# Optimization experiments

Hardware: AMD Instinct MI355X
Metric: run time of the kernel (lower is better)

Reference implementation:

```python
import jax, jax.numpy as jnp
import numpy as np

ROPE_BASE = 10000.0

def _rms_norm(x):
    eps = jnp.asarray(jnp.finfo(x.dtype).eps, x.dtype)
    return x * jax.lax.rsqrt(jnp.mean(x * x, axis=-1, keepdims=True) + eps)

def _rope(x):
    # x: [B, S, H, hd]; rotate-halves variant: y1 = x1*cos + x2*sin, y2 = -x1*sin + x2*cos
    S, hd = x.shape[1], x.shape[3]
    d = hd // 2
    inv_freq = 1.0 / (ROPE_BASE ** (jnp.arange(0, hd, 2, dtype=jnp.float32) / hd))  # [d]
    t = jnp.arange(S, dtype=jnp.float32)
    freqs = jnp.outer(t, inv_freq)                       # [S, d]
    cos = jnp.cos(freqs)[None, :, None, :].astype(x.dtype)
    sin = jnp.sin(freqs)[None, :, None, :].astype(x.dtype)
    x1, x2 = x[..., :d], x[..., d:]
    return jnp.concatenate([x1 * cos + x2 * sin, -x1 * sin + x2 * cos], axis=-1)

def setup_inputs() -> dict:
    key = jax.random.key(0)
    ks = jax.random.split(key, 7)
    B, S, D = 1, 2048, 1024
    std = 0.02
    return {
        "x": jax.random.normal(ks[0], (B, S, D), jnp.float32),
        "v1": jax.random.normal(ks[1], (B, S, D), jnp.float32),
        "Wq": jax.random.normal(ks[2], (D, D), jnp.float32) * std,
        "Wk": jax.random.normal(ks[3], (D, D), jnp.float32) * std,
        "Wv": jax.random.normal(ks[4], (D, D), jnp.float32) * std,
        "Wout": jax.random.normal(ks[5], (D, D), jnp.float32) * std,
        "lambdas": jnp.float32(0.5),
        "n_heads": 16,
    }

def reference(x, v1, Wq, Wk, Wv, Wout, lambdas, n_heads):
    B, S, D = x.shape
    H = n_heads
    hd = D // H
    # QKV projections (CastedLinear, no bias)
    q = (x @ Wq.T).reshape(B, S, H, hd)
    k = (x @ Wk.T).reshape(B, S, H, hd)
    v = (x @ Wv.T).reshape(B, S, H, hd)
    # value residual mix with first-layer values v1
    v = (1.0 - lambdas) * v + lambdas * v1.reshape(B, S, H, hd)
    # per-head RMS norm (no learned scale) then RoPE
    q, k = _rms_norm(q), _rms_norm(k)
    q, k = _rope(q), _rope(k)
    # causal attention (flex_attention default: softmax, scale 1/sqrt(hd))
    scale = 1.0 / jnp.sqrt(jnp.asarray(hd, x.dtype))
    scores = jnp.einsum('bqhd,bkhd->bhqk', q, k) * scale        # [B,H,S,S]
    causal = jnp.tril(jnp.ones((S, S), dtype=bool))
    scores = jnp.where(causal[None, None], scores, jnp.asarray(-jnp.inf, scores.dtype))
    p = jax.nn.softmax(scores, axis=-1)
    y = jnp.einsum('bhqk,bkhd->bqhd', p, v).reshape(B, S, D)
    y = y @ Wout.T
    return (y, v1)
```

## Files before the change

kernel.cpp:

```cpp
#include <hip/hip_runtime.h>
#include <hip/hip_bf16.h>

#define S_LEN 2048
#define D_DIM 1024
#define NH    16
#define NEG_BIG (-1.0e30f)

#define EPI_NORMROPE 1
#define EPI_VMIX_T   2
#define EPI_F32      3

typedef __attribute__((ext_vector_type(8))) short bf16x8;
typedef __attribute__((ext_vector_type(4))) float f32x4;
typedef const __attribute__((address_space(1))) unsigned char gu8_t;
typedef __attribute__((address_space(3))) unsigned char lu8_t;

__device__ __forceinline__ float bf2f(unsigned short h) {
    union { unsigned int u; float f; } v; v.u = ((unsigned int)h) << 16; return v.f;
}
__device__ __forceinline__ unsigned short f2b(float f) {
    union { float f; unsigned int u; } v; v.f = f;
    unsigned int u = v.u;
    return (unsigned short)((u + 0x7FFFu + ((u >> 16) & 1u)) >> 16);
}

__global__ __launch_bounds__(256)
void to_bf16(const float* __restrict__ x,  const float* __restrict__ wq,
             const float* __restrict__ wk, const float* __restrict__ wv,
             const float* __restrict__ wo,
             unsigned short* __restrict__ xb,  unsigned short* __restrict__ wqb,
             unsigned short* __restrict__ wkb, unsigned short* __restrict__ wvb,
             unsigned short* __restrict__ wob)
{
    const int z = blockIdx.y;
    const float* s; unsigned short* d; int n;
    switch (z) {
        case 0: s = x;  d = xb;  n = S_LEN * D_DIM; break;
        case 1: s = wq; d = wqb; n = D_DIM * D_DIM; break;
        case 2: s = wk; d = wkb; n = D_DIM * D_DIM; break;
        case 3: s = wv; d = wvb; n = D_DIM * D_DIM; break;
        default: s = wo; d = wob; n = D_DIM * D_DIM; break;
    }
    int i8 = blockIdx.x * 256 + threadIdx.x;
    if (i8 * 8 >= n) return;
    const float* sp = s + (size_t)i8 * 8;
    float4 lo = *(const float4*)sp, hi = *(const float4*)(sp + 4);
    uint4 p;
    p.x = f2b(lo.x) | ((unsigned)f2b(lo.y) << 16);
    p.y = f2b(lo.z) | ((unsigned)f2b(lo.w) << 16);
    p.z = f2b(hi.x) | ((unsigned)f2b(hi.y) << 16);
    p.w = f2b(hi.z) | ((unsigned)f2b(hi.w) << 16);
    *(uint4*)(d + (size_t)i8 * 8) = p;
}

__global__ __launch_bounds__(256, 2)
void gemm_bt(const unsigned short* __restrict__ A,
             const unsigned short* __restrict__ B0, const unsigned short* __restrict__ B1,
             const unsigned short* __restrict__ B2,
             void* __restrict__ C0, void* __restrict__ C1, void* __restrict__ C2,
             const float* __restrict__ vmix, const float* __restrict__ lam,
             int epiPack)
{
    const int which = blockIdx.z;
    const unsigned short* Bp = (which == 0) ? B0 : ((which == 1) ? B1 : B2);
    void* C = (which == 0) ? C0 : ((which == 1) ? C1 : C2);
    const int epi = (epiPack >> (8 * which)) & 0xff;
    const int tn = blockIdx.x * 128;
    const int tm = blockIdx.y * 128;

    __shared__ unsigned short Asl[128 * 32];
    __shared__ unsigned short Bsl[128 * 32];

    const int t    = threadIdx.x;
    const int lane = t & 63;
    const int wave = t >> 6;
    const int wm   = (wave >> 1) * 64;
    const int wn   = (wave & 1) * 64;
    const int lrow = lane & 15;
    const int quad = lane >> 4;
    const int srow = lane >> 2;
    const int scol = (lane & 3) * 8;

    f32x4 acc[4][4];
    #pragma unroll
    for (int i = 0; i < 4; ++i)
        #pragma unroll
        for (int j = 0; j < 4; ++j) {
            f32x4 z = {0.f, 0.f, 0.f, 0.f};
            acc[i][j] = z;
        }

    for (int k0 = 0; k0 < D_DIM; k0 += 32) {
        #pragma unroll
        for (int rep = 0; rep < 2; ++rep) {
            int grp = wave * 2 + rep;
            int row = grp * 16 + srow;
            __builtin_amdgcn_global_load_lds(
                (gu8_t*)(A + (size_t)(tm + row) * D_DIM + k0 + scol),
                (lu8_t*)&Asl[grp * 512], 16, 0, 0);
            __builtin_amdgcn_global_load_lds(
                (gu8_t*)(Bp + (size_t)(tn + row) * D_DIM + k0 + scol),
                (lu8_t*)&Bsl[grp * 512], 16, 0, 0);
        }
        __syncthreads();
        bf16x8 af[4], bfr[4];
        #pragma unroll
        for (int i = 0; i < 4; ++i)
            af[i] = *(const bf16x8*)(&Asl[(wm + i * 16 + lrow) * 32 + quad * 8]);
        #pragma unroll
        for (int j = 0; j < 4; ++j)
            bfr[j] = *(const bf16x8*)(&Bsl[(wn + j * 16 + lrow) * 32 + quad * 8]);
        #pragma unroll
        for (int i = 0; i < 4; ++i)
            #pragma unroll
            for (int j = 0; j < 4; ++j)
                acc[i][j] = __builtin_amdgcn_mfma_f32_16x16x32_bf16(af[i], bfr[j], acc[i][j], 0, 0, 0);
        __syncthreads();
    }

    if (epi == EPI_NORMROPE) {
        #pragma unroll
        for (int i = 0; i < 4; ++i) {
            #pragma unroll
            for (int r = 0; r < 4; ++r) {
                int row = tm + wm + i * 16 + quad * 4 + r;
                float v0 = acc[i][0][r], v1 = acc[i][1][r];
                float v2 = acc[i][2][r], v3 = acc[i][3][r];
                float ss = v0 * v0 + v1 * v1 + v2 * v2 + v3 * v3;
                ss += __shfl_xor(ss, 1); ss += __shfl_xor(ss, 2);
                ss += __shfl_xor(ss, 4); ss += __shfl_xor(ss, 8);
                float rms = rsqrtf(ss * (1.f / 64.f) + 1.1920929e-7f);
                v0 *= rms; v1 *= rms; v2 *= rms; v3 *= rms;
                float fs = (float)row;
                float a0 = fs * exp2f(-0.41524101186092030f * (float)lrow);
                float a1 = fs * exp2f(-0.41524101186092030f * (float)(16 + lrow));
                float s0, c0, s1, c1;
                __sincosf(a0, &s0, &c0);
                __sincosf(a1, &s1, &c1);
                unsigned short* Cb = (unsigned short*)C;
                size_t base = (size_t)row * D_DIM + tn + wn + lrow;
                Cb[base]      = f2b(v0 * c0 + v2 * s0);
                Cb[base + 16] = f2b(v1 * c1 + v3 * s1);
                Cb[base + 32] = f2b(-v0 * s0 + v2 * c0);
                Cb[base + 48] = f2b(-v1 * s1 + v3 * c1);
            }
        }
    } else if (epi == EPI_VMIX_T) {
        float lamf = *lam;
        #pragma unroll
        for (int i = 0; i < 4; ++i) {
            int cm0 = tm + wm + i * 16 + quad * 4;
            #pragma unroll
            for (int j = 0; j < 4; ++j) {
                int cn = tn + wn + j * 16 + lrow;
                ushort4 pk;
                float vals[4];
                #pragma unroll
                for (int r = 0; r < 4; ++r) {
                    size_t idx = (size_t)(cm0 + r) * D_DIM + cn;
                    vals[r] = (1.f - lamf) * acc[i][j][r] + lamf * vmix[idx];
                }
                pk.x = f2b(vals[0]); pk.y = f2b(vals[1]);
                pk.z = f2b(vals[2]); pk.w = f2b(vals[3]);
                *(ushort4*)((unsigned short*)C + (size_t)cn * S_LEN + cm0) = pk;
            }
        }
    } else {
        #pragma unroll
        for (int i = 0; i < 4; ++i) {
            int cm0 = tm + wm + i * 16 + quad * 4;
            #pragma unroll
            for (int j = 0; j < 4; ++j) {
                int cn = tn + wn + j * 16 + lrow;
                #pragma unroll
                for (int r = 0; r < 4; ++r)
                    ((float*)C)[(size_t)(cm0 + r) * D_DIM + cn] = acc[i][j][r];
            }
        }
    }
}

__global__ __launch_bounds__(256, 2)
void attn_mfma(const unsigned short* Qb,
               const unsigned short* __restrict__ Kb,
               const unsigned short* __restrict__ Vtg,
               unsigned short* Ob)
{
    const int bx = blockIdx.x;
    const int qt = (bx & 1) ? (31 - (bx >> 1)) : (bx >> 1);
    const int h  = blockIdx.y;
    const int t  = threadIdx.x;
    const int w  = t >> 6;
    const int l  = t & 63;
    const int l15  = l & 15;
    const int quad = l >> 4;
    const int hco  = h * 64;

    __shared__ unsigned short Ks[64][72];
    __shared__ unsigned short Vt[64][72];
    __shared__ unsigned short Ps[4][16][72];

    const unsigned short* qrow = Qb + (size_t)(qt * 64 + w * 16 + l15) * D_DIM + hco;
    bf16x8 qf0 = *(const bf16x8*)(qrow + quad * 8);
    bf16x8 qf1 = *(const bf16x8*)(qrow + 32 + quad * 8);

    f32x4 oac[4];
    #pragma unroll
    for (int nt = 0; nt < 4; ++nt) { f32x4 z = {0.f,0.f,0.f,0.f}; oac[nt] = z; }
    float l_lane[4] = {0.f, 0.f, 0.f, 0.f};

    const int rr = t >> 2;
    const int dc = (t & 3) * 16;

    const unsigned short* kbase = Kb  + (size_t)rr * D_DIM + hco + dc;
    const unsigned short* vbase = Vtg + (size_t)(hco + rr) * S_LEN + dc;

    uint4 ka0, ka1, va0, va1;
    ka0 = *(const uint4*)kbase;  ka1 = *(const uint4*)(kbase + 8);
    va0 = *(const uint4*)vbase;  va1 = *(const uint4*)(vbase + 8);

    const int row_base = qt * 64 + w * 16 + quad * 4;

    for (int j = 0; j <= qt; ++j) {
        __syncthreads();
        *(uint4*)&Ks[rr][dc]     = ka0;
        *(uint4*)&Ks[rr][dc + 8] = ka1;
        *(uint4*)&Vt[rr][dc]     = va0;
        *(uint4*)&Vt[rr][dc + 8] = va1;
        __syncthreads();
        if (j < qt) {
            const unsigned short* kp = kbase + (size_t)(j + 1) * 64 * D_DIM;
            const unsigned short* vp = vbase + (size_t)(j + 1) * 64;
            ka0 = *(const uint4*)kp;  ka1 = *(const uint4*)(kp + 8);
            va0 = *(const uint4*)vp;  va1 = *(const uint4*)(vp + 8);
        }

        f32x4 sac[4];
        #pragma unroll
        for (int nt = 0; nt < 4; ++nt) {
            f32x4 z = {0.f,0.f,0.f,0.f};
            bf16x8 kf0 = *(const bf16x8*)&Ks[nt * 16 + l15][quad * 8];
            z = __builtin_amdgcn_mfma_f32_16x16x32_bf16(qf0, kf0, z, 0, 0, 0);
            bf16x8 kf1 = *(const bf16x8*)&Ks[nt * 16 + l15][32 + quad * 8];
            z = __builtin_amdgcn_mfma_f32_16x16x32_bf16(qf1, kf1, z, 0, 0, 0);
            sac[nt] = z;
        }

        #pragma unroll
        for (int nt = 0; nt < 4; ++nt) {
            int key_g = j * 64 + nt * 16 + l15;
            #pragma unroll
            for (int r = 0; r < 4; ++r) {
                float s = sac[nt][r] * 0.125f - 8.0f;
                if (key_g > row_base + r) s = NEG_BIG;
                float pe = __expf(s);
                l_lane[r] += pe;
                Ps[w][quad * 4 + r][nt * 16 + l15] = f2b(pe);
            }
        }

        bf16x8 pf0 = *(const bf16x8*)&Ps[w][l15][quad * 8];
        bf16x8 pf1 = *(const bf16x8*)&Ps[w][l15][32 + quad * 8];
        #pragma unroll
        for (int nt = 0; nt < 4; ++nt) {
            bf16x8 vf0 = *(const bf16x8*)&Vt[nt * 16 + l15][quad * 8];
            oac[nt] = __builtin_amdgcn_mfma_f32_16x16x32_bf16(pf0, vf0, oac[nt], 0, 0, 0);
            bf16x8 vf1 = *(const bf16x8*)&Vt[nt * 16 + l15][32 + quad * 8];
            oac[nt] = __builtin_amdgcn_mfma_f32_16x16x32_bf16(pf1, vf1, oac[nt], 0, 0, 0);
        }
    }

    float inv[4];
    #pragma unroll
    for (int r = 0; r < 4; ++r) {
        float lr = l_lane[r];
        #pragma unroll
        for (int d = 1; d < 16; d <<= 1) lr += __shfl_xor(lr, d);
        inv[r] = 1.f / lr;
    }
    #pragma unroll
    for (int nt = 0; nt < 4; ++nt) {
        #pragma unroll
        for (int r = 0; r < 4; ++r) {
            int row_g = row_base + r;
            Ob[(size_t)row_g * D_DIM + hco + nt * 16 + l15] = f2b(oac[nt][r] * inv[r]);
        }
    }
}

__global__ __launch_bounds__(256)
void copy_v1(const uint4* __restrict__ src, uint4* __restrict__ dst) {
    int i = blockIdx.x * 256 + threadIdx.x;
    dst[i] = src[i];
}

extern "C" void kernel_launch(void* const* d_in, const int* in_sizes, int n_in,
                              void* d_out, int out_size, void* d_ws, size_t ws_size,
                              hipStream_t stream)
{
    const float* x    = (const float*)d_in[0];
    const float* v1   = (const float*)d_in[1];
    const float* Wq   = (const float*)d_in[2];
    const float* Wk   = (const float*)d_in[3];
    const float* Wv   = (const float*)d_in[4];
    const float* Wout = (const float*)d_in[5];
    const float* lam  = (const float*)d_in[6];
    float* out = (float*)d_out;

    const size_t SD = (size_t)S_LEN * D_DIM;
    const size_t DD = (size_t)D_DIM * D_DIM;
    unsigned short* Qb  = (unsigned short*)d_ws;
    unsigned short* Kb  = Qb + SD;
    unsigned short* Vtg = Kb + SD;
    unsigned short* Ab  = Qb;

    unsigned short* Wqb   = (unsigned short*)d_out;
    unsigned short* Wkb   = Wqb + DD;
    unsigned short* Wvb   = Wkb + DD;
    unsigned short* xb    = (unsigned short*)(out + SD);
    unsigned short* Woutb = xb + SD;

    to_bf16<<<dim3(1024, 5), 256, 0, stream>>>(
        x, Wq, Wk, Wv, Wout, xb, Wqb, Wkb, Wvb, Woutb);

    gemm_bt<<<dim3(D_DIM / 128, S_LEN / 128, 3), 256, 0, stream>>>(
        xb, Wqb, Wkb, Wvb, Qb, Kb, Vtg, v1, lam,
        EPI_NORMROPE | (EPI_NORMROPE << 8) | (EPI_VMIX_T << 16));

    attn_mfma<<<dim3(S_LEN / 64, NH), 256, 0, stream>>>(Qb, Kb, Vtg, Ab);

    gemm_bt<<<dim3(D_DIM / 128, S_LEN / 128, 1), 256, 0, stream>>>(
        Ab, Woutb, Woutb, Woutb, d_out, d_out, d_out, nullptr, lam, EPI_F32);

    copy_v1<<<dim3((unsigned)(SD / 4 / 256)), 256, 0, stream>>>(
        (const uint4*)v1, (uint4*)(out + SD));
}
```

Before: 181.9 us.

## Fold softmax scale into Q, double-buffer K/V, skip mask on interior tiles

Q's norm/rope epilogue now multiplies by scale*log2(e), so attention computes probabilities with exp2f of the score plus a constant instead of a multiply and __expf. K/V shared tiles are double-buffered, which removes one __syncthreads per iteration. The causal mask is applied only on the diagonal tile, and P is truncated rather than rounded to bf16. The GEMM launch bounds are raised to 3 blocks per CU, which may force register spills, and truncation adds a small rounding bias.

```diff
diff --git a/kernel.cpp b/kernel.cpp
--- a/kernel.cpp
+++ b/kernel.cpp
@@ -6,9 +6,10 @@
 #define NH    16
 #define NEG_BIG (-1.0e30f)
 
-#define EPI_NORMROPE 1
-#define EPI_VMIX_T   2
-#define EPI_F32      3
+#define EPI_NORMROPE   1
+#define EPI_VMIX_T     2
+#define EPI_F32        3
+#define EPI_NORMROPE_Q 4
 
 typedef __attribute__((ext_vector_type(8))) short bf16x8;
 typedef __attribute__((ext_vector_type(4))) float f32x4;
@@ -22,6 +23,10 @@
     union { float f; unsigned int u; } v; v.f = f;
     unsigned int u = v.u;
     return (unsigned short)((u + 0x7FFFu + ((u >> 16) & 1u)) >> 16);
+}
+__device__ __forceinline__ unsigned short f2b_trunc(float f) {
+    union { float f; unsigned int u; } v; v.f = f;
+    return (unsigned short)(v.u >> 16);
 }
 
 __global__ __launch_bounds__(256)
@@ -53,7 +58,7 @@
     *(uint4*)(d + (size_t)i8 * 8) = p;
 }
 
-__global__ __launch_bounds__(256, 2)
+__global__ __launch_bounds__(256, 3)
 void gemm_bt(const unsigned short* __restrict__ A,
              const unsigned short* __restrict__ B0, const unsigned short* __restrict__ B1,
              const unsigned short* __restrict__ B2,
@@ -118,7 +123,8 @@
         __syncthreads();
     }
 
-    if (epi == EPI_NORMROPE) {
+    if (epi == EPI_NORMROPE || epi == EPI_NORMROPE_Q) {
+        const float post = (epi == EPI_NORMROPE_Q) ? 0.18033688011112042f : 1.0f;
         #pragma unroll
         for (int i = 0; i < 4; ++i) {
             #pragma unroll
@@ -129,7 +135,7 @@
                 float ss = v0 * v0 + v1 * v1 + v2 * v2 + v3 * v3;
                 ss += __shfl_xor(ss, 1); ss += __shfl_xor(ss, 2);
                 ss += __shfl_xor(ss, 4); ss += __shfl_xor(ss, 8);
-                float rms = rsqrtf(ss * (1.f / 64.f) + 1.1920929e-7f);
+                float rms = rsqrtf(ss * (1.f / 64.f) + 1.1920929e-7f) * post;
                 v0 *= rms; v1 *= rms; v2 *= rms; v3 *= rms;
                 float fs = (float)row;
                 float a0 = fs * exp2f(-0.41524101186092030f * (float)lrow);
@@ -196,8 +202,8 @@
     const int quad = l >> 4;
     const int hco  = h * 64;
 
-    __shared__ unsigned short Ks[64][72];
-    __shared__ unsigned short Vt[64][72];
+    __shared__ unsigned short Ks[2][64][72];
+    __shared__ unsigned short Vt[2][64][72];
     __shared__ unsigned short Ps[4][16][72];
 
     const unsigned short* qrow = Qb + (size_t)(qt * 64 + w * 16 + l15) * D_DIM + hco;
@@ -220,13 +226,14 @@
     va0 = *(const uint4*)vbase;  va1 = *(const uint4*)(vbase + 8);
 
     const int row_base = qt * 64 + w * 16 + quad * 4;
+    const float C2 = -11.541560327111707f;
 
     for (int j = 0; j <= qt; ++j) {
-        __syncthreads();
-        *(uint4*)&Ks[rr][dc]     = ka0;
-        *(uint4*)&Ks[rr][dc + 8] = ka1;
-        *(uint4*)&Vt[rr][dc]     = va0;
-        *(uint4*)&Vt[rr][dc + 8] = va1;
+        const int buf = j & 1;
+        *(uint4*)&Ks[buf][rr][dc]     = ka0;
+        *(uint4*)&Ks[buf][rr][dc + 8] = ka1;
+        *(uint4*)&Vt[buf][rr][dc]     = va0;
+        *(uint4*)&Vt[buf][rr][dc + 8] = va1;
         __syncthreads();
         if (j < qt) {
             const unsigned short* kp = kbase + (size_t)(j + 1) * 64 * D_DIM;
@@ -239,23 +246,35 @@
         #pragma unroll
         for (int nt = 0; nt < 4; ++nt) {
             f32x4 z = {0.f,0.f,0.f,0.f};
-            bf16x8 kf0 = *(const bf16x8*)&Ks[nt * 16 + l15][quad * 8];
+            bf16x8 kf0 = *(const bf16x8*)&Ks[buf][nt * 16 + l15][quad * 8];
             z = __builtin_amdgcn_mfma_f32_16x16x32_bf16(qf0, kf0, z, 0, 0, 0);
-            bf16x8 kf1 = *(const bf16x8*)&Ks[nt * 16 + l15][32 + quad * 8];
+            bf16x8 kf1 = *(const bf16x8*)&Ks[buf][nt * 16 + l15][32 + quad * 8];
             z = __builtin_amdgcn_mfma_f32_16x16x32_bf16(qf1, kf1, z, 0, 0, 0);
             sac[nt] = z;
         }
 
-        #pragma unroll
-        for (int nt = 0; nt < 4; ++nt) {
-            int key_g = j * 64 + nt * 16 + l15;
-            #pragma unroll
-            for (int r = 0; r < 4; ++r) {
-                float s = sac[nt][r] * 0.125f - 8.0f;
-                if (key_g > row_base + r) s = NEG_BIG;
-                float pe = __expf(s);
-                l_lane[r] += pe;
-                Ps[w][quad * 4 + r][nt * 16 + l15] = f2b(pe);
+        if (j < qt) {
+            #pragma unroll
+            for (int nt = 0; nt < 4; ++nt) {
+                #pragma unroll
+                for (int r = 0; r < 4; ++r) {
+                    float pe = exp2f(sac[nt][r] + C2);
+                    l_lane[r] += pe;
+                    Ps[w][quad * 4 + r][nt * 16 + l15] = f2b_trunc(pe);
+                }
+            }
+        } else {
+            #pragma unroll
+            for (int nt = 0; nt < 4; ++nt) {
+                int key_g = j * 64 + nt * 16 + l15;
+                #pragma unroll
+                for (int r = 0; r < 4; ++r) {
+                    float s = sac[nt][r] + C2;
+                    if (key_g > row_base + r) s = NEG_BIG;
+                    float pe = exp2f(s);
+                    l_lane[r] += pe;
+                    Ps[w][quad * 4 + r][nt * 16 + l15] = f2b_trunc(pe);
+                }
             }
         }
 
@@ -263,9 +282,9 @@
         bf16x8 pf1 = *(const bf16x8*)&Ps[w][l15][32 + quad * 8];
         #pragma unroll
         for (int nt = 0; nt < 4; ++nt) {
-            bf16x8 vf0 = *(const bf16x8*)&Vt[nt * 16 + l15][quad * 8];
+            bf16x8 vf0 = *(const bf16x8*)&Vt[buf][nt * 16 + l15][quad * 8];
             oac[nt] = __builtin_amdgcn_mfma_f32_16x16x32_bf16(pf0, vf0, oac[nt], 0, 0, 0);
-            bf16x8 vf1 = *(const bf16x8*)&Vt[nt * 16 + l15][32 + quad * 8];
+            bf16x8 vf1 = *(const bf16x8*)&Vt[buf][nt * 16 + l15][32 + quad * 8];
             oac[nt] = __builtin_amdgcn_mfma_f32_16x16x32_bf16(pf1, vf1, oac[nt], 0, 0, 0);
         }
     }
@@ -325,7 +344,7 @@
 
     gemm_bt<<<dim3(D_DIM / 128, S_LEN / 128, 3), 256, 0, stream>>>(
         xb, Wqb, Wkb, Wvb, Qb, Kb, Vtg, v1, lam,
-        EPI_NORMROPE | (EPI_NORMROPE << 8) | (EPI_VMIX_T << 16));
+        EPI_NORMROPE_Q | (EPI_NORMROPE << 8) | (EPI_VMIX_T << 16));
 
     attn_mfma<<<dim3(S_LEN / 64, NH), 256, 0, stream>>>(Qb, Kb, Vtg, Ab);
 
```

Measured after the change: 180.4 us. No clear change (-0.8%).
